# Kernel tuning notes

Measured on AMD Instinct MI355X. Metric: run time of the kernel, lower is better.

Reference implementation:

```python
import jax, jax.numpy as jnp
import numpy as np

GRID_DIM = 7  # margin = 0, so each grid cell is a disjoint (H//g, W//g) tile


def setup_inputs() -> dict:
    key = jax.random.key(0)
    k1, k2 = jax.random.split(key)
    B, H, W, C = 8, 224, 224, 256
    NQ = 64
    images = jax.random.normal(k1, (B, H, W, C), dtype=jnp.float32)
    queries = jax.random.normal(k2, (NQ, C), dtype=jnp.float32)
    return {"images": images, "queries": queries}


def reference(images, queries):
    # images: [B, H, W, C]; queries: [NQ, C]
    B, H, W, C = images.shape
    g = GRID_DIM
    hs, ws = H // g, W // g  # tile size per grid cell (margin = 0)
    # Crop all g*g cells at once: [B, g, hs, g, ws, C] -> [B, g*g, L, C]
    # Cell index n = i*g + j (i over height, j over width) matches the
    # original positions ordering (pos[0] -> height, pos[1] -> width).
    regions = images.reshape(B, g, hs, g, ws, C)
    regions = regions.transpose(0, 1, 3, 2, 4, 5).reshape(B, g * g, hs * ws, C)
    # keras.layers.Attention default: unscaled dot-product + softmax.
    scores = jnp.einsum('qc,bnlc->bnql', queries, regions)  # [B, g*g, NQ, L]
    attn = jax.nn.softmax(scores, axis=-1)
    out = jnp.einsum('bnql,bnlc->bnqc', attn, regions)      # [B, g*g, NQ, C]
    return out
```

## Files before the change

kernel.cpp:

```cpp
#include <hip/hip_runtime.h>

typedef _Float16 half8 __attribute__((ext_vector_type(8)));
typedef _Float16 half4 __attribute__((ext_vector_type(4)));
typedef __fp16   fp16x2 __attribute__((ext_vector_type(2)));
typedef float f32x4  __attribute__((ext_vector_type(4)));

#define DEVI __device__ __forceinline__

constexpr int Bc = 8;
constexpr int Hc = 224;
constexpr int Wc = 224;
constexpr int Cc = 256;
constexpr int NQ = 64;
constexpr int TS = 32;
constexpr int Lc = TS * TS;
constexpr int KL = 64;
constexpr int NT = Lc / KL;

DEVI int subidx(int l, int c) {
  return ((((l >> 2) << 4) | (c >> 4)) << 6) | (((l & 3) << 4) | (c & 15));
}

DEVI uint ldsoff(const void* p) {
  return (uint)(uintptr_t)(const __attribute__((address_space(3))) char*)p;
}

union PKU { fp16x2 h; uint u; };
DEVI uint pkrtz(float a, float b) { PKU x; x.h = __builtin_amdgcn_cvt_pkrtz(a, b); return x.u; }

__global__ __launch_bounds__(256, 2) void attn_cells(
    const float* __restrict__ img,
    const float* __restrict__ qry,
    float* __restrict__ out)
{
  __shared__ _Float16 Rlds[2][KL * Cc];
  __shared__ _Float16 Plds[4][16 * KL];
  __shared__ float    Slds[NQ];
  __shared__ float    Llds[NQ];

  const int tid  = threadIdx.x;
  const int w    = tid >> 6;
  const int lane = tid & 63;
  const int lp   = lane & 15;
  const int gq   = lane >> 4;

  const int bn = blockIdx.x;
  const int b  = bn / 49;
  const int n  = bn % 49;
  const int i0 = n / 7, j0 = n % 7;

  const long cellbase = (((long)b * Hc + i0 * TS) * Wc + j0 * TS) * Cc;

  int goff[8], lds_off[8];
  #pragma unroll
  for (int s = 0; s < 8; ++s) {
    int G   = s * 256 + tid;
    int blk = G >> 3, sub = G & 7;
    int l   = ((blk >> 4) << 2) | ((sub >> 1) & 3);
    int c   = ((blk & 15) << 4) | ((sub & 1) << 3);
    int y   = l >> 5, x = l & 31;
    goff[s]    = (y * Wc + x) * Cc + c;
    lds_off[s] = G << 3;
  }

  half8 bq[8];
  {
    const int qrow = (w << 4) | lp;
    #pragma unroll
    for (int kc = 0; kc < 8; ++kc) {
      const float* qp = &qry[qrow * Cc + kc * 32 + gq * 8];
      f32x4 lo = *(const f32x4*)qp;
      f32x4 hi = *(const f32x4*)(qp + 4);
      half8 h;
      #pragma unroll
      for (int j = 0; j < 4; ++j) { h[j] = (_Float16)lo[j]; h[j + 4] = (_Float16)hi[j]; }
      bq[kc] = h;
    }
  }

  f32x4 acc[4][4];
  #pragma unroll
  for (int qb = 0; qb < 4; ++qb)
    #pragma unroll
    for (int cb = 0; cb < 4; ++cb) acc[qb][cb] = f32x4{0.f, 0.f, 0.f, 0.f};

  float mrun = -3.0e38f;
  float lsum = 0.0f;

  {
    const float* gb = img + cellbase;
    #pragma unroll
    for (int s = 0; s < 8; ++s) {
      f32x4 lo = *(const f32x4*)&gb[goff[s]];
      f32x4 hi = *(const f32x4*)&gb[goff[s] + 4];
      uint4 pk;
      pk.x = pkrtz(lo[0], lo[1]); pk.y = pkrtz(lo[2], lo[3]);
      pk.z = pkrtz(hi[0], hi[1]); pk.w = pkrtz(hi[2], hi[3]);
      *(uint4*)&Rlds[0][lds_off[s]] = pk;
    }
  }
  __syncthreads();

  const uint trlane = (uint)(gq * 4096 + w * 512 +
                             ((((lp >> 2) << 4) | ((lp & 3) << 2)) << 1));

  for (int t = 0; t < NT; ++t) {
    const int pb = t & 1;
    const _Float16* Rbuf = &Rlds[pb][0];
    const uint trbase = ldsoff(Rbuf) + trlane;

    f32x4 stg[16];
    if (t + 1 < NT) {
      const float* gb = img + cellbase + (long)(t + 1) * (2 * Wc * Cc);
      #pragma unroll
      for (int s = 0; s < 8; ++s) {
        stg[2 * s]     = *(const f32x4*)&gb[goff[s]];
        stg[2 * s + 1] = *(const f32x4*)&gb[goff[s] + 4];
      }
    }

    f32x4 sv[4];
    #pragma unroll
    for (int lb = 0; lb < 4; ++lb) sv[lb] = f32x4{0.f, 0.f, 0.f, 0.f};
    #pragma unroll
    for (int kc = 0; kc < 8; ++kc) {
      #pragma unroll
      for (int lb = 0; lb < 4; ++lb) {
        half8 a = *(const half8*)&Rbuf[subidx(lb * 16 + lp, kc * 32 + gq * 8)];
        sv[lb] = __builtin_amdgcn_mfma_f32_16x16x32_f16(a, bq[kc], sv[lb], 0, 0, 0);
      }
    }

    float cmax = sv[0][0];
    #pragma unroll
    for (int lb = 0; lb < 4; ++lb)
      #pragma unroll
      for (int r = 0; r < 4; ++r) cmax = fmaxf(cmax, sv[lb][r]);
    cmax = fmaxf(cmax, __shfl_xor(cmax, 16));
    cmax = fmaxf(cmax, __shfl_xor(cmax, 32));

    float mnew  = fmaxf(mrun, cmax);
    float scale = __expf(mrun - mnew);

    float ps = 0.0f;
    float pv[4][4];
    #pragma unroll
    for (int lb = 0; lb < 4; ++lb)
      #pragma unroll
      for (int r = 0; r < 4; ++r) {
        float p = __expf(sv[lb][r] - mnew);
        pv[lb][r] = p; ps += p;
      }
    ps += __shfl_xor(ps, 16);
    ps += __shfl_xor(ps, 32);
    lsum = lsum * scale + ps;
    mrun = mnew;

    {
      char* Pw = (char*)&Plds[w][0];
      #pragma unroll
      for (int lb = 0; lb < 4; ++lb) {
        uint lo = pkrtz(pv[lb][0], pv[lb][1]);
        uint hi = pkrtz(pv[lb][2], pv[lb][3]);
        int base = lp * 128 + lb * 32 + gq * 8;
        int swz  = (lp & 7) << 4;
        *(uint*)(Pw + ((base ^ swz)))     = lo;
        *(uint*)(Pw + ((base ^ swz) + 4)) = hi;
      }
      if (lane < 16) Slds[w * 16 + lp] = scale;
    }

    __syncthreads();

    #pragma unroll
    for (int qb = 0; qb < 4; ++qb) {
      f32x4 sc = *(const f32x4*)&Slds[qb * 16 + gq * 4];
      #pragma unroll
      for (int cb = 0; cb < 4; ++cb) acc[qb][cb] *= sc;
    }

    #pragma unroll
    for (int kc = 0; kc < 2; ++kc) {
      half8 pa[4];
      #pragma unroll
      for (int qb = 0; qb < 4; ++qb) {
        const char* Pr = (const char*)&Plds[qb][0];
        int off = (lp * 128 + gq * 16 + kc * 64) ^ ((lp & 7) << 4);
        pa[qb] = *(const half8*)(Pr + off);
      }
      half4 tr[4][2];
      #pragma unroll
      for (int cb = 0; cb < 4; ++cb) {
        #pragma unroll
        for (int u = 0; u < 2; ++u) {
          asm volatile("ds_read_b64_tr_b16 %0, %1 offset:%2"
                       : "=v"(tr[cb][u])
                       : "v"(trbase), "i"(kc * 16384 + u * 2048 + cb * 128));
        }
      }
      asm volatile("s_waitcnt lgkmcnt(0)" ::: "memory");
      __builtin_amdgcn_sched_barrier(0);

      #pragma unroll
      for (int qb = 0; qb < 4; ++qb)
        #pragma unroll
        for (int cb = 0; cb < 4; ++cb) {
          half8 bv = __builtin_shufflevector(tr[cb][0], tr[cb][1], 0, 1, 2, 3, 4, 5, 6, 7);
          acc[qb][cb] = __builtin_amdgcn_mfma_f32_16x16x32_f16(pa[qb], bv, acc[qb][cb], 0, 0, 0);
        }
    }

    if (t + 1 < NT) {
      _Float16* Rn = &Rlds[pb ^ 1][0];
      #pragma unroll
      for (int s = 0; s < 8; ++s) {
        uint4 pk;
        pk.x = pkrtz(stg[2 * s][0], stg[2 * s][1]);
        pk.y = pkrtz(stg[2 * s][2], stg[2 * s][3]);
        pk.z = pkrtz(stg[2 * s + 1][0], stg[2 * s + 1][1]);
        pk.w = pkrtz(stg[2 * s + 1][2], stg[2 * s + 1][3]);
        *(uint4*)&Rn[lds_off[s]] = pk;
      }
    }

    __syncthreads();
  }

  if (lane < 16) Llds[w * 16 + lp] = lsum;
  __syncthreads();

  float* ob = out + (long)bn * NQ * Cc;
  #pragma unroll
  for (int qb = 0; qb < 4; ++qb) {
    f32x4 lv = *(const f32x4*)&Llds[qb * 16 + gq * 4];
    #pragma unroll
    for (int r = 0; r < 4; ++r) {
      const float iv = 1.0f / lv[r];
      const int q = qb * 16 + gq * 4 + r;
      #pragma unroll
      for (int cb = 0; cb < 4; ++cb) {
        const int c = w * 64 + cb * 16 + lp;
        ob[q * Cc + c] = acc[qb][cb][r] * iv;
      }
    }
  }
}

extern "C" void kernel_launch(void* const* d_in, const int* in_sizes, int n_in,
                              void* d_out, int out_size, void* d_ws, size_t ws_size,
                              hipStream_t stream) {
  const float* img = (const float*)d_in[0];
  const float* qry = (const float*)d_in[1];
  float* outp      = (float*)d_out;
  dim3 grid(Bc * 49), block(256);
  attn_cells<<<grid, block, 0, stream>>>(img, qry, outp);
}
```

Before: 96.97 us.

## Split each cell's sequence into two halves and combine partial softmax results

Each cell's 1024-position sequence is processed by two blocks that write fp16 partial accumulators plus running max and sum into a workspace, and a second kernel merges them with log-sum-exp rescaling. This doubles the block count to fill more of the GPU. The next-tile prefetch now converts and stores into LDS immediately instead of holding staged registers across compute, reducing register pressure. It adds workspace traffic, a second launch, fp16 rounding of partials, and less load/compute overlap.

```diff
diff --git a/kernel.cpp b/kernel.cpp
--- a/kernel.cpp
+++ b/kernel.cpp
@@ -17,6 +17,9 @@
 constexpr int KL = 64;
 constexpr int NT = Lc / KL;
 
+constexpr long PSTRIDE = 64 * 256 * 2 + 64 * 4 + 64 * 4;
+constexpr long WS_NEED = 784 * PSTRIDE;
+
 DEVI int subidx(int l, int c) {
   return ((((l >> 2) << 4) | (c >> 4)) << 6) | (((l & 3) << 4) | (c & 15));
 }
@@ -27,11 +30,15 @@
 
 union PKU { fp16x2 h; uint u; };
 DEVI uint pkrtz(float a, float b) { PKU x; x.h = __builtin_amdgcn_cvt_pkrtz(a, b); return x.u; }
+union HBU { _Float16 h; ushort u; };
+DEVI ushort hbits(float x) { HBU v; v.h = (_Float16)x; return v.u; }
 
 __global__ __launch_bounds__(256, 2) void attn_cells(
     const float* __restrict__ img,
     const float* __restrict__ qry,
-    float* __restrict__ out)
+    float* __restrict__ out,
+    char* __restrict__ wsp,
+    int splt)
 {
   __shared__ _Float16 Rlds[2][KL * Cc];
   __shared__ _Float16 Plds[4][16 * KL];
@@ -44,7 +51,12 @@
   const int lp   = lane & 15;
   const int gq   = lane >> 4;
 
-  const int bn = blockIdx.x;
+  const int bx = blockIdx.x;
+  const int bn = splt ? (bx >> 1) : bx;
+  const int h  = splt ? (bx & 1)  : 0;
+  const int tbeg = h * 8;
+  const int tend = tbeg + (splt ? 8 : NT);
+
   const int b  = bn / 49;
   const int n  = bn % 49;
   const int i0 = n / 7, j0 = n % 7;
@@ -71,10 +83,10 @@
       const float* qp = &qry[qrow * Cc + kc * 32 + gq * 8];
       f32x4 lo = *(const f32x4*)qp;
       f32x4 hi = *(const f32x4*)(qp + 4);
-      half8 h;
-      #pragma unroll
-      for (int j = 0; j < 4; ++j) { h[j] = (_Float16)lo[j]; h[j + 4] = (_Float16)hi[j]; }
-      bq[kc] = h;
+      half8 hh;
+      #pragma unroll
+      for (int j = 0; j < 4; ++j) { hh[j] = (_Float16)lo[j]; hh[j + 4] = (_Float16)hi[j]; }
+      bq[kc] = hh;
     }
   }
 
@@ -88,7 +100,7 @@
   float lsum = 0.0f;
 
   {
-    const float* gb = img + cellbase;
+    const float* gb = img + cellbase + (long)tbeg * (2 * Wc * Cc);
     #pragma unroll
     for (int s = 0; s < 8; ++s) {
       f32x4 lo = *(const f32x4*)&gb[goff[s]];
@@ -104,18 +116,22 @@
   const uint trlane = (uint)(gq * 4096 + w * 512 +
                              ((((lp >> 2) << 4) | ((lp & 3) << 2)) << 1));
 
-  for (int t = 0; t < NT; ++t) {
+  for (int t = tbeg; t < tend; ++t) {
     const int pb = t & 1;
     const _Float16* Rbuf = &Rlds[pb][0];
     const uint trbase = ldsoff(Rbuf) + trlane;
 
-    f32x4 stg[16];
-    if (t + 1 < NT) {
+    if (t + 1 < tend) {
       const float* gb = img + cellbase + (long)(t + 1) * (2 * Wc * Cc);
+      _Float16* Rn = &Rlds[pb ^ 1][0];
       #pragma unroll
       for (int s = 0; s < 8; ++s) {
-        stg[2 * s]     = *(const f32x4*)&gb[goff[s]];
-        stg[2 * s + 1] = *(const f32x4*)&gb[goff[s] + 4];
+        f32x4 lo = *(const f32x4*)&gb[goff[s]];
+        f32x4 hi = *(const f32x4*)&gb[goff[s] + 4];
+        uint4 pk;
+        pk.x = pkrtz(lo[0], lo[1]); pk.y = pkrtz(lo[2], lo[3]);
+        pk.z = pkrtz(hi[0], hi[1]); pk.w = pkrtz(hi[2], hi[3]);
+        *(uint4*)&Rn[lds_off[s]] = pk;
       }
     }
 
@@ -210,39 +226,77 @@
         }
     }
 
-    if (t + 1 < NT) {
-      _Float16* Rn = &Rlds[pb ^ 1][0];
-      #pragma unroll
-      for (int s = 0; s < 8; ++s) {
-        uint4 pk;
-        pk.x = pkrtz(stg[2 * s][0], stg[2 * s][1]);
-        pk.y = pkrtz(stg[2 * s][2], stg[2 * s][3]);
-        pk.z = pkrtz(stg[2 * s + 1][0], stg[2 * s + 1][1]);
-        pk.w = pkrtz(stg[2 * s + 1][2], stg[2 * s + 1][3]);
-        *(uint4*)&Rn[lds_off[s]] = pk;
-      }
-    }
-
     __syncthreads();
   }
 
-  if (lane < 16) Llds[w * 16 + lp] = lsum;
-  __syncthreads();
-
-  float* ob = out + (long)bn * NQ * Cc;
+  if (splt) {
+    char* pbase = wsp + (long)bx * PSTRIDE;
+    #pragma unroll
+    for (int qb = 0; qb < 4; ++qb)
+      #pragma unroll
+      for (int r = 0; r < 4; ++r) {
+        const int q = qb * 16 + gq * 4 + r;
+        #pragma unroll
+        for (int cb = 0; cb < 4; ++cb) {
+          const int c = w * 64 + cb * 16 + lp;
+          *(ushort*)(pbase + (q * 256 + c) * 2) = hbits(acc[qb][cb][r]);
+        }
+      }
+    if (lane < 16) {
+      const int q = w * 16 + lp;
+      *(float*)(pbase + 32768 + q * 4) = mrun;
+      *(float*)(pbase + 33024 + q * 4) = lsum;
+    }
+  } else {
+    if (lane < 16) Llds[w * 16 + lp] = lsum;
+    __syncthreads();
+    float* ob = out + (long)bn * NQ * Cc;
+    #pragma unroll
+    for (int qb = 0; qb < 4; ++qb) {
+      f32x4 lv = *(const f32x4*)&Llds[qb * 16 + gq * 4];
+      #pragma unroll
+      for (int r = 0; r < 4; ++r) {
+        const float iv = 1.0f / lv[r];
+        const int q = qb * 16 + gq * 4 + r;
+        #pragma unroll
+        for (int cb = 0; cb < 4; ++cb) {
+          const int c = w * 64 + cb * 16 + lp;
+          ob[q * Cc + c] = acc[qb][cb][r] * iv;
+        }
+      }
+    }
+  }
+}
+
+__global__ __launch_bounds__(256) void combine_halves(
+    const char* __restrict__ ws, float* __restrict__ out)
+{
+  const int cell = blockIdx.x >> 1;
+  const int qh   = blockIdx.x & 1;
+  const int t    = threadIdx.x;
+
+  const char* p0 = ws + (long)(cell * 2 + 0) * PSTRIDE;
+  const char* p1 = ws + (long)(cell * 2 + 1) * PSTRIDE;
+  float* ob = out + (long)cell * (NQ * Cc);
+
   #pragma unroll
-  for (int qb = 0; qb < 4; ++qb) {
-    f32x4 lv = *(const f32x4*)&Llds[qb * 16 + gq * 4];
-    #pragma unroll
-    for (int r = 0; r < 4; ++r) {
-      const float iv = 1.0f / lv[r];
-      const int q = qb * 16 + gq * 4 + r;
-      #pragma unroll
-      for (int cb = 0; cb < 4; ++cb) {
-        const int c = w * 64 + cb * 16 + lp;
-        ob[q * Cc + c] = acc[qb][cb][r] * iv;
-      }
-    }
+  for (int v = 0; v < 4; ++v) {
+    const int f = qh * 8192 + v * 2048 + t * 8;
+    const int q = f >> 8;
+    const float m0 = *(const float*)(p0 + 32768 + q * 4);
+    const float m1 = *(const float*)(p1 + 32768 + q * 4);
+    const float l0 = *(const float*)(p0 + 33024 + q * 4);
+    const float l1 = *(const float*)(p1 + 33024 + q * 4);
+    const float M  = fmaxf(m0, m1);
+    const float a0 = __expf(m0 - M), a1 = __expf(m1 - M);
+    const float inv = 1.0f / (a0 * l0 + a1 * l1);
+
+    half8 x0 = *(const half8*)(p0 + (long)f * 2);
+    half8 x1 = *(const half8*)(p1 + (long)f * 2);
+    float* o = ob + f;
+    #pragma unroll
+    for (int j = 0; j < 8; ++j)
+      o[j] = (a0 * (float)x0[j] + a1 * (float)x1[j]) * inv;
   }
 }
 
@@ -252,6 +306,10 @@
   const float* img = (const float*)d_in[0];
   const float* qry = (const float*)d_in[1];
   float* outp      = (float*)d_out;
-  dim3 grid(Bc * 49), block(256);
-  attn_cells<<<grid, block, 0, stream>>>(img, qry, outp);
-}
+  if (ws_size >= (size_t)WS_NEED) {
+    attn_cells<<<dim3(Bc * 49 * 2), dim3(256), 0, stream>>>(img, qry, outp, (char*)d_ws, 1);
+    combine_halves<<<dim3(Bc * 49 * 2), dim3(256), 0, stream>>>((const char*)d_ws, outp);
+  } else {
+    attn_cells<<<dim3(Bc * 49), dim3(256), 0, stream>>>(img, qry, outp, (char*)d_ws, 0);
+  }
+}
```

Measured after the change: 114.1 us. 17.7% more time.
